# Kernel optimization log

Measured on AMD Instinct MI355X. Metric: run time of the kernel, lower is better.

Reference implementation:

```python
import jax, jax.numpy as jnp
import numpy as np

BATCH = 8192
FEATS = 4096
RATE = 0.1
ANNEAL = 0.5 + 0.1  # self.anneal = 0.5 + anneal


def setup_inputs() -> dict:
    key = jax.random.key(0)
    k1, k2 = jax.random.split(key)
    inputs = jax.random.normal(k1, (BATCH, FEATS), dtype=jnp.float32)
    # standard-normal draws, one per feature (replaces the serial map_fn RNG)
    noise = jax.random.normal(k2, (FEATS,), dtype=jnp.float32)
    return {"inputs": inputs, "noise": noise}


def reference(inputs, noise):
    # SegDropout (training path), agg_method='mean', noise_type='gaussian'
    F = inputs.shape[-1]
    x_agg = jnp.mean(inputs, axis=0)                      # [F] batch-wise aggregate
    x_min = jnp.min(x_agg)
    x_max = jnp.max(x_agg)
    # quantize each feature's aggregate into one of F+1 integer bins
    bins = (F * (x_agg - x_min) / (x_max - x_min)).astype(jnp.int32)  # [F], values in [0, F]
    # unique_with_counts + gather(counts, idx) == histogram lookup per feature
    counts_per_bin = jnp.bincount(bins, length=F + 1)      # [F+1]
    counts = counts_per_bin[bins].astype(inputs.dtype)     # [F] count of each feature's bin
    dr = RATE ** (1.0 / (ANNEAL * counts))                 # annealed per-bin dropout rate
    dr = jnp.where(counts == 1.0, jnp.asarray(RATE, inputs.dtype), dr)
    sigma = jnp.sqrt(dr / (1.0 - dr))                      # [F]
    # multiplicative Gaussian noise ~ N(1, sigma) per feature
    return inputs * (1.0 + sigma * noise)
```

## Files before the change

kernel.cpp:

```cpp
#include <hip/hip_runtime.h>

#define BATCH 8192
#define FEATS 4096
#define CHUNKS 128
#define ROWS_PER_CHUNK (BATCH / CHUNKS)
#define SROWS 16
#define NRBLK (FEATS / 256)

typedef float v4f __attribute__((ext_vector_type(4)));


__global__ __launch_bounds__(256) void colsum_part(const float* __restrict__ in,
                                                   double* __restrict__ partials) {
    const int colBase = blockIdx.x * 1024 + threadIdx.x * 4;
    const int row0 = blockIdx.y * ROWS_PER_CHUNK;
    const float4* p = (const float4*)in + (size_t)row0 * (FEATS / 4) + (colBase >> 2);
    double a0 = 0.0, a1 = 0.0, a2 = 0.0, a3 = 0.0;
#pragma unroll 16
    for (int r = 0; r < ROWS_PER_CHUNK; ++r) {
        float4 v = p[(size_t)r * (FEATS / 4)];
        a0 += (double)v.x; a1 += (double)v.y; a2 += (double)v.z; a3 += (double)v.w;
    }
    double* dst = partials + (size_t)blockIdx.y * FEATS + colBase;
    dst[0] = a0; dst[1] = a1; dst[2] = a2; dst[3] = a3;
}

__global__ __launch_bounds__(256) void reduce_mean(const double* __restrict__ partials,
                                                   double* __restrict__ means,
                                                   double* __restrict__ bmin,
                                                   double* __restrict__ bmax) {
    const int c = blockIdx.x * 256 + threadIdx.x;
    double s = 0.0;
#pragma unroll 8
    for (int k = 0; k < CHUNKS; ++k) s += partials[(size_t)k * FEATS + c];
    const double m = s * (1.0 / (double)BATCH);
    means[c] = m;

    double lmin = m, lmax = m;
#pragma unroll
    for (int off = 32; off > 0; off >>= 1) {
        lmin = fmin(lmin, __shfl_down(lmin, off));
        lmax = fmax(lmax, __shfl_down(lmax, off));
    }
    __shared__ double smin[4], smax[4];
    const int wv = threadIdx.x >> 6;
    if ((threadIdx.x & 63) == 0) { smin[wv] = lmin; smax[wv] = lmax; }
    __syncthreads();
    if (threadIdx.x == 0) {
        bmin[blockIdx.x] = fmin(fmin(smin[0], smin[1]), fmin(smin[2], smin[3]));
        bmax[blockIdx.x] = fmax(fmax(smax[0], smax[1]), fmax(smax[2], smax[3]));
    }
}

__global__ __launch_bounds__(1024) void config_kernel(const double* __restrict__ means,
                                                      const double* __restrict__ bmin,
                                                      const double* __restrict__ bmax,
                                                      const float* __restrict__ noise,
                                                      float* __restrict__ scale) {
    __shared__ unsigned s_hist[FEATS + 1];
    __shared__ double s_mm[2];
    const int tid = threadIdx.x;

    if (tid == 0) {
        double a = bmin[0], b = bmax[0];
        for (int i = 1; i < NRBLK; ++i) { a = fmin(a, bmin[i]); b = fmax(b, bmax[i]); }
        s_mm[0] = a; s_mm[1] = b;
    }
    for (int i = tid; i < FEATS + 1; i += 1024) s_hist[i] = 0;
    __syncthreads();

    const double xmin = s_mm[0];
    const double denom = s_mm[1] - xmin;

    int binr[4];
#pragma unroll
    for (int k = 0; k < 4; ++k) {
        int c = tid + k * 1024;
        double b = ((double)FEATS * (means[c] - xmin)) / denom;
        int bi = (int)b;
        binr[k] = bi;
        atomicAdd(&s_hist[bi], 1u);
    }
    __syncthreads();

    const double K = -2.302585092994045684017991454684364208;
#pragma unroll
    for (int k = 0; k < 4; ++k) {
        int c = tid + k * 1024;
        unsigned cnt = s_hist[binr[k]];
        double dr = (cnt == 1u) ? 0.1 : exp(K / (0.6 * (double)cnt));
        double sg = sqrt(dr / (1.0 - dr));
        scale[c] = (float)(1.0 + sg * (double)noise[c]);
    }
}

__global__ __launch_bounds__(256) void scale_kernel(const float4* __restrict__ in,
                                                    const float4* __restrict__ scale,
                                                    float4* __restrict__ out) {
    const int col = (blockIdx.x & 3) * 256 + threadIdx.x;
    const int row0 = (blockIdx.x >> 2) * SROWS;
    const float4 s = scale[col];
    const float4* pin = in + (size_t)row0 * (FEATS / 4) + col;
    float4* pout = out + (size_t)row0 * (FEATS / 4) + col;
#pragma unroll
    for (int r = 0; r < SROWS; ++r) {
        float4 v = pin[(size_t)r * (FEATS / 4)];
        v.x *= s.x; v.y *= s.y; v.z *= s.z; v.w *= s.w;
        v4f nv = {v.x, v.y, v.z, v.w};
        __builtin_nontemporal_store(nv, (v4f*)&pout[(size_t)r * (FEATS / 4)]);
    }
}

extern "C" void kernel_launch(void* const* d_in, const int* in_sizes, int n_in,
                              void* d_out, int out_size, void* d_ws, size_t ws_size,
                              hipStream_t stream) {
    const float* in = (const float*)d_in[0];
    const float* noise = (const float*)d_in[1];
    float* out = (float*)d_out;
    double* partials = (double*)d_ws;
    double* means = partials + (size_t)CHUNKS * FEATS;
    double* bmin = means + FEATS;
    double* bmax = bmin + NRBLK;
    float* scale = (float*)(bmax + NRBLK);

    dim3 g1(4, CHUNKS);
    colsum_part<<<g1, 256, 0, stream>>>(in, partials);
    reduce_mean<<<NRBLK, 256, 0, stream>>>(partials, means, bmin, bmax);
    config_kernel<<<1, 1024, 0, stream>>>(means, bmin, bmax, noise, scale);
    scale_kernel<<<4 * (BATCH / SROWS), 256, 0, stream>>>(
        (const float4*)in, (const float4*)scale, (float4*)out);
}
```

Before: 260.6 us.

## Fuse mean reduction and config into one kernel via last-block counter

Merges the reduce_mean and config_kernel launches into a single kernel. The last block to finish, detected with an atomic counter, builds the histogram and computes the scales. The mean reduction is split into 64 blocks, each with four K-slices reduced through shared memory, and colsum uses 256 row chunks with a smaller unroll. This removes one kernel launch and gap and widens the partial-sum stage, at the cost of threadfences, an atomic, and a config phase running on 256 threads instead of 1024.

Result: slower. 276.0 us (+5.9%).

```diff
diff --git a/kernel.cpp b/kernel.cpp
--- a/kernel.cpp
+++ b/kernel.cpp
@@ -2,21 +2,25 @@
 
 #define BATCH 8192
 #define FEATS 4096
-#define CHUNKS 128
+#define CHUNKS 256
 #define ROWS_PER_CHUNK (BATCH / CHUNKS)
 #define SROWS 16
-#define NRBLK (FEATS / 256)
+#define RBLK 64
+#define KSLICES 4
+#define KPER (CHUNKS / KSLICES)
 
 typedef float v4f __attribute__((ext_vector_type(4)));
 
 
 __global__ __launch_bounds__(256) void colsum_part(const float* __restrict__ in,
-                                                   double* __restrict__ partials) {
+                                                   double* __restrict__ partials,
+                                                   unsigned* __restrict__ counter) {
+    if (blockIdx.x == 0 && blockIdx.y == 0 && threadIdx.x == 0) *counter = 0u;
     const int colBase = blockIdx.x * 1024 + threadIdx.x * 4;
     const int row0 = blockIdx.y * ROWS_PER_CHUNK;
     const float4* p = (const float4*)in + (size_t)row0 * (FEATS / 4) + (colBase >> 2);
     double a0 = 0.0, a1 = 0.0, a2 = 0.0, a3 = 0.0;
-#pragma unroll 16
+#pragma unroll 8
     for (int r = 0; r < ROWS_PER_CHUNK; ++r) {
         float4 v = p[(size_t)r * (FEATS / 4)];
         a0 += (double)v.x; a1 += (double)v.y; a2 += (double)v.z; a3 += (double)v.w;
@@ -25,58 +29,66 @@
     dst[0] = a0; dst[1] = a1; dst[2] = a2; dst[3] = a3;
 }
 
-__global__ __launch_bounds__(256) void reduce_mean(const double* __restrict__ partials,
-                                                   double* __restrict__ means,
-                                                   double* __restrict__ bmin,
-                                                   double* __restrict__ bmax) {
-    const int c = blockIdx.x * 256 + threadIdx.x;
+__global__ __launch_bounds__(256) void reduce_config(const double* __restrict__ partials,
+                                                     const float* __restrict__ noise,
+                                                     double* __restrict__ means,
+                                                     double* __restrict__ bmin,
+                                                     double* __restrict__ bmax,
+                                                     float* __restrict__ scale,
+                                                     unsigned* __restrict__ counter) {
+    const int t = threadIdx.x;
+    const int cLocal = t & 63;
+    const int ks = t >> 6;
+    const int c = blockIdx.x * 64 + cLocal;
+
     double s = 0.0;
 #pragma unroll 8
-    for (int k = 0; k < CHUNKS; ++k) s += partials[(size_t)k * FEATS + c];
-    const double m = s * (1.0 / (double)BATCH);
-    means[c] = m;
+    for (int k = 0; k < KPER; ++k)
+        s += partials[(size_t)(ks * KPER + k) * FEATS + c];
 
-    double lmin = m, lmax = m;
+    __shared__ double sred[KSLICES][64];
+    sred[ks][cLocal] = s;
+    __syncthreads();
+
+    if (ks == 0) {
+        double m = ((sred[0][cLocal] + sred[1][cLocal]) + sred[2][cLocal]) + sred[3][cLocal];
+        m *= (1.0 / (double)BATCH);
+        means[c] = m;
+        double lmin = m, lmax = m;
 #pragma unroll
-    for (int off = 32; off > 0; off >>= 1) {
-        lmin = fmin(lmin, __shfl_down(lmin, off));
-        lmax = fmax(lmax, __shfl_down(lmax, off));
+        for (int off = 32; off > 0; off >>= 1) {
+            lmin = fmin(lmin, __shfl_down(lmin, off));
+            lmax = fmax(lmax, __shfl_down(lmax, off));
+        }
+        if (cLocal == 0) { bmin[blockIdx.x] = lmin; bmax[blockIdx.x] = lmax; }
     }
-    __shared__ double smin[4], smax[4];
-    const int wv = threadIdx.x >> 6;
-    if ((threadIdx.x & 63) == 0) { smin[wv] = lmin; smax[wv] = lmax; }
+    __threadfence();
     __syncthreads();
-    if (threadIdx.x == 0) {
-        bmin[blockIdx.x] = fmin(fmin(smin[0], smin[1]), fmin(smin[2], smin[3]));
-        bmax[blockIdx.x] = fmax(fmax(smax[0], smax[1]), fmax(smax[2], smax[3]));
-    }
-}
 
-__global__ __launch_bounds__(1024) void config_kernel(const double* __restrict__ means,
-                                                      const double* __restrict__ bmin,
-                                                      const double* __restrict__ bmax,
-                                                      const float* __restrict__ noise,
-                                                      float* __restrict__ scale) {
+    __shared__ unsigned isLast;
+    if (t == 0) isLast = (atomicAdd(counter, 1u) == RBLK - 1) ? 1u : 0u;
+    __syncthreads();
+    if (!isLast) return;
+    __threadfence();
+
     __shared__ unsigned s_hist[FEATS + 1];
     __shared__ double s_mm[2];
-    const int tid = threadIdx.x;
-
-    if (tid == 0) {
+    if (t == 0) {
         double a = bmin[0], b = bmax[0];
-        for (int i = 1; i < NRBLK; ++i) { a = fmin(a, bmin[i]); b = fmax(b, bmax[i]); }
+        for (int i = 1; i < RBLK; ++i) { a = fmin(a, bmin[i]); b = fmax(b, bmax[i]); }
         s_mm[0] = a; s_mm[1] = b;
     }
-    for (int i = tid; i < FEATS + 1; i += 1024) s_hist[i] = 0;
+    for (int i = t; i < FEATS + 1; i += 256) s_hist[i] = 0;
     __syncthreads();
 
     const double xmin = s_mm[0];
     const double denom = s_mm[1] - xmin;
 
-    int binr[4];
+    int binr[16];
 #pragma unroll
-    for (int k = 0; k < 4; ++k) {
-        int c = tid + k * 1024;
-        double b = ((double)FEATS * (means[c] - xmin)) / denom;
+    for (int k = 0; k < 16; ++k) {
+        int c2 = t + k * 256;
+        double b = ((double)FEATS * (means[c2] - xmin)) / denom;
         int bi = (int)b;
         binr[k] = bi;
         atomicAdd(&s_hist[bi], 1u);
@@ -85,12 +97,12 @@
 
     const double K = -2.302585092994045684017991454684364208;
 #pragma unroll
-    for (int k = 0; k < 4; ++k) {
-        int c = tid + k * 1024;
+    for (int k = 0; k < 16; ++k) {
+        int c2 = t + k * 256;
         unsigned cnt = s_hist[binr[k]];
         double dr = (cnt == 1u) ? 0.1 : exp(K / (0.6 * (double)cnt));
         double sg = sqrt(dr / (1.0 - dr));
-        scale[c] = (float)(1.0 + sg * (double)noise[c]);
+        scale[c2] = (float)(1.0 + sg * (double)noise[c2]);
     }
 }
 
@@ -120,13 +132,13 @@
     double* partials = (double*)d_ws;
     double* means = partials + (size_t)CHUNKS * FEATS;
     double* bmin = means + FEATS;
-    double* bmax = bmin + NRBLK;
-    float* scale = (float*)(bmax + NRBLK);
+    double* bmax = bmin + RBLK;
+    float* scale = (float*)(bmax + RBLK);
+    unsigned* counter = (unsigned*)(scale + FEATS);
 
     dim3 g1(4, CHUNKS);
-    colsum_part<<<g1, 256, 0, stream>>>(in, partials);
-    reduce_mean<<<NRBLK, 256, 0, stream>>>(partials, means, bmin, bmax);
-    config_kernel<<<1, 1024, 0, stream>>>(means, bmin, bmax, noise, scale);
+    colsum_part<<<g1, 256, 0, stream>>>(in, partials, counter);
+    reduce_config<<<RBLK, 256, 0, stream>>>(partials, noise, means, bmin, bmax, scale, counter);
     scale_kernel<<<4 * (BATCH / SROWS), 256, 0, stream>>>(
         (const float4*)in, (const float4*)scale, (float4*)out);
 }
```
